# Kernel tuning notes

Hardware: AMD Instinct MI355X
Metric: run time of the kernel (lower is better)

The kernel has to match this reference:

```python
import jax, jax.numpy as jnp
import numpy as np

B, N, K, H, L = 2, 1024, 48, 128, 3
SCALE = 30.0


def _gelu(x):
    # torch.nn.GELU default is the exact erf formulation
    return jax.nn.gelu(x, approximate=False)


def _ln(x, g, b, eps=1e-5):
    mu = jnp.mean(x, axis=-1, keepdims=True)
    var = jnp.mean((x - mu) ** 2, axis=-1, keepdims=True)
    return g * (x - mu) * jax.lax.rsqrt(var + eps) + b


def _gather_nodes(nodes, idx):
    # nodes: [B,N,H], idx: [B,N,K] -> [B,N,K,H]
    b, n, k = idx.shape
    flat = idx.reshape(b, n * k)
    g = jnp.take_along_axis(nodes, flat[:, :, None], axis=1)
    return g.reshape(b, n, k, nodes.shape[-1])


def setup_inputs() -> dict:
    key = jax.random.key(0)
    ks = jax.random.split(key, 16)

    def w(k, shape, fan_in):
        return jax.random.normal(k, shape, jnp.float32) / np.sqrt(fan_in).astype(np.float32)

    kp = jax.random.split(ks[5], 9)
    inp = {
        "h_V": jax.random.normal(ks[0], (B, N, H), jnp.float32),
        "h_E": jax.random.normal(ks[1], (B, N, K, H), jnp.float32),
        "E_idx": jax.random.randint(ks[2], (B, N, K), 0, N),
        "mask_V": jnp.ones((B, N), jnp.float32),
        "mask_attend": jnp.ones((B, N, K), jnp.float32),
        # message MLP (node update): W1 [3H->H], W2, W3
        "W1": w(kp[0], (L, 3 * H, H), 3 * H), "b1": jnp.zeros((L, H), jnp.float32),
        "W2": w(kp[1], (L, H, H), H), "b2": jnp.zeros((L, H), jnp.float32),
        "W3": w(kp[2], (L, H, H), H), "b3": jnp.zeros((L, H), jnp.float32),
        # message MLP (edge update): W11 [3H->H], W12, W13
        "W11": w(kp[3], (L, 3 * H, H), 3 * H), "b11": jnp.zeros((L, H), jnp.float32),
        "W12": w(kp[4], (L, H, H), H), "b12": jnp.zeros((L, H), jnp.float32),
        "W13": w(kp[5], (L, H, H), H), "b13": jnp.zeros((L, H), jnp.float32),
        # position-wise FFN: H -> 4H -> H
        "Win": w(kp[6], (L, H, 4 * H), H), "bin_": jnp.zeros((L, 4 * H), jnp.float32),
        "Wout": w(kp[7], (L, 4 * H, H), 4 * H), "bout": jnp.zeros((L, H), jnp.float32),
        # LayerNorms
        "g1": jnp.ones((L, H), jnp.float32), "be1": jnp.zeros((L, H), jnp.float32),
        "g2": jnp.ones((L, H), jnp.float32), "be2": jnp.zeros((L, H), jnp.float32),
        "g3": jnp.ones((L, H), jnp.float32), "be3": jnp.zeros((L, H), jnp.float32),
    }
    return inp


def reference(h_V, h_E, E_idx, mask_V, mask_attend,
              W1, b1, W2, b2, W3, b3,
              W11, b11, W12, b12, W13, b13,
              Win, bin_, Wout, bout,
              g1, be1, g2, be2, g3, be3):
    # Stack of L EncLayers (eval mode, dropout = identity).
    for l in range(L):
        # --- node update: gather neighbors, concat, 3-layer MLP message ---
        hVn = _gather_nodes(h_V, E_idx)                        # [B,N,K,H]
        hVe = jnp.broadcast_to(h_V[:, :, None, :], hVn.shape)  # [B,N,K,H]
        h_EV = jnp.concatenate([hVe, h_E, hVn], axis=-1)       # [B,N,K,3H]
        m = _gelu(h_EV @ W1[l] + b1[l])
        m = _gelu(m @ W2[l] + b2[l])
        m = m @ W3[l] + b3[l]
        m = mask_attend[..., None] * m
        dh = jnp.sum(m, axis=-2) / SCALE                       # masked sum aggregate
        h_V = _ln(h_V + dh, g1[l], be1[l])
        dh = _gelu(h_V @ Win[l] + bin_[l]) @ Wout[l] + bout[l]
        h_V = _ln(h_V + dh, g2[l], be2[l])
        h_V = mask_V[..., None] * h_V
        # --- edge update ---
        hVn = _gather_nodes(h_V, E_idx)
        hVe = jnp.broadcast_to(h_V[:, :, None, :], hVn.shape)
        h_EV = jnp.concatenate([hVe, h_E, hVn], axis=-1)
        m = _gelu(h_EV @ W11[l] + b11[l])
        m = _gelu(m @ W12[l] + b12[l])
        m = m @ W13[l] + b13[l]
        h_E = _ln(h_E + m, g3[l], be3[l])
    return h_V, h_E
```

## Files before the change

kernel.cpp:

```cpp
#include <hip/hip_runtime.h>
#include <hip/hip_bf16.h>
#include <math.h>

#define BB 2
#define NN 1024
#define HH 128
#define LL 3
#define SY 136
#define SH 520
#define SX 136
#define SM 132

typedef __attribute__((ext_vector_type(8))) short s8v;
typedef __attribute__((ext_vector_type(4))) float f4v;
typedef unsigned short u16;

static __device__ __forceinline__ u16 f2bf(float x) {
  union { float f; unsigned u; } v; v.f = x;
  unsigned r = v.u + 0x7FFFu + ((v.u >> 16) & 1u);
  return (u16)(r >> 16);
}
static __device__ __forceinline__ float geluf(float x) {
  float x2 = x * x;
  float u2 = x * (1.5957691216f + 0.0713548163f * x2);
  float e = __expf(u2);
  float d = __builtin_amdgcn_rcpf(e + 1.0f);
  return x - x * d;
}

static __device__ __forceinline__ void gemm48k128(const u16* __restrict__ A,
                                                  const u16* __restrict__ Wt,
                                                  int wave, int lane, f4v acc[3][2]) {
  const int g = lane >> 4, q = lane & 15;
  s8v B0[4], B1[4];
  const u16* wb0 = Wt + (wave * 32 + q) * 128 + g * 8;
  const u16* wb1 = wb0 + 16 * 128;
#pragma unroll
  for (int t = 0; t < 4; ++t) { B0[t] = *(const s8v*)(wb0 + t * 32); B1[t] = *(const s8v*)(wb1 + t * 32); }
#pragma unroll
  for (int t = 0; t < 4; ++t) {
    const u16* Ab = A + t * 32 + g * 8;
    s8v a0 = *(const s8v*)(Ab + q * SY);
    s8v a1 = *(const s8v*)(Ab + (16 + q) * SY);
    s8v a2 = *(const s8v*)(Ab + (32 + q) * SY);
    acc[0][0] = __builtin_amdgcn_mfma_f32_16x16x32_bf16(a0, B0[t], acc[0][0], 0, 0, 0);
    acc[0][1] = __builtin_amdgcn_mfma_f32_16x16x32_bf16(a0, B1[t], acc[0][1], 0, 0, 0);
    acc[1][0] = __builtin_amdgcn_mfma_f32_16x16x32_bf16(a1, B0[t], acc[1][0], 0, 0, 0);
    acc[1][1] = __builtin_amdgcn_mfma_f32_16x16x32_bf16(a1, B1[t], acc[1][1], 0, 0, 0);
    acc[2][0] = __builtin_amdgcn_mfma_f32_16x16x32_bf16(a2, B0[t], acc[2][0], 0, 0, 0);
    acc[2][1] = __builtin_amdgcn_mfma_f32_16x16x32_bf16(a2, B1[t], acc[2][1], 0, 0, 0);
  }
}

static __device__ __forceinline__ void zero_acc(f4v acc[3][2]) {
#pragma unroll
  for (int rt = 0; rt < 3; ++rt)
#pragma unroll
    for (int c = 0; c < 2; ++c) acc[rt][c] = (f4v){0.f, 0.f, 0.f, 0.f};
}

static __device__ __forceinline__ void store_act(const f4v acc[3][2], u16* __restrict__ Y,
                                                 int wave, int lane, const float* __restrict__ bias) {
  const int g = lane >> 4, q = lane & 15;
#pragma unroll
  for (int c = 0; c < 2; ++c) {
    const int col = wave * 32 + c * 16 + q;
    const float bv = bias[col];
#pragma unroll
    for (int rt = 0; rt < 3; ++rt)
#pragma unroll
      for (int r = 0; r < 4; ++r) {
        const int row = rt * 16 + g * 4 + r;
        Y[row * SY + col] = f2bf(geluf(acc[rt][c][r] + bv));
      }
  }
}

static __device__ __forceinline__ void stage_hE(u16* __restrict__ dst, const float* __restrict__ src,
                                                int tid) {
  const float4* hEr = (const float4*)src;
#pragma unroll
  for (int p = 0; p < 6; ++p) {
    int i = tid + p * 256; int row = i >> 5, c = i & 31;
    float4 v = hEr[row * 32 + c];
    uint2 pk;
    pk.x = (unsigned)f2bf(v.x) | ((unsigned)f2bf(v.y) << 16);
    pk.y = (unsigned)f2bf(v.z) | ((unsigned)f2bf(v.w) << 16);
    *(uint2*)(dst + row * SY + c * 4) = pk;
  }
}

__global__ void conv_weights(const float* __restrict__ W1, const float* __restrict__ W2,
                             const float* __restrict__ W3, const float* __restrict__ W11,
                             const float* __restrict__ W12, const float* __restrict__ W13,
                             const float* __restrict__ Win, const float* __restrict__ Wout,
                             const float* __restrict__ hV,
                             u16* __restrict__ W1bT, u16* __restrict__ W2t,
                             u16* __restrict__ W3t, u16* __restrict__ W11bT,
                             u16* __restrict__ W12t, u16* __restrict__ W13t,
                             u16* __restrict__ Wint, u16* __restrict__ Woutt,
                             u16* __restrict__ PRE, u16* __restrict__ hv0bf) {
  const int tid = blockIdx.x * blockDim.x + threadIdx.x;
  const int nt = gridDim.x * blockDim.x;
  for (int i = tid; i < LL * 128 * 128; i += nt) {
    int l = i >> 14, rem = i & 16383;
    int k = rem >> 7, n = rem & 127;
    const int o = (l * 128 + n) * 128 + k;
    W1bT [o] = f2bf(W1 [l * 49152 + (128 + k) * 128 + n]);
    W11bT[o] = f2bf(W11[l * 49152 + (128 + k) * 128 + n]);
    W2t  [o] = f2bf(W2 [i]);
    W3t  [o] = f2bf(W3 [i]);
    W12t [o] = f2bf(W12[i]);
    W13t [o] = f2bf(W13[i]);
  }
  for (int i = tid; i < LL * 128 * 128; i += nt) {
    int l = i >> 14, rem = i & 16383;
    int k = rem >> 7, n = rem & 127;
    const int o = (l * 128 + n) * 128 + k;
    const int s = l * 16384 + k * 128 + n;
    W2t [o] = f2bf(W2 [s]);
    W3t [o] = f2bf(W3 [s]);
    W12t[o] = f2bf(W12[s]);
    W13t[o] = f2bf(W13[s]);
    const int ln = (l + 1 == LL) ? 0 : l + 1;
    PRE[l * 65536 + (0 * 128 + n) * 128 + k] = f2bf(W11[l * 49152 + k * 128 + n]);
    PRE[l * 65536 + (1 * 128 + n) * 128 + k] = f2bf(W11[l * 49152 + (256 + k) * 128 + n]);
    PRE[l * 65536 + (2 * 128 + n) * 128 + k] = f2bf(W1 [ln * 49152 + k * 128 + n]);
    PRE[l * 65536 + (3 * 128 + n) * 128 + k] = f2bf(W1 [ln * 49152 + (256 + k) * 128 + n]);
  }
  for (int i = tid; i < LL * 128 * 512; i += nt) {
    int l = i / (128 * 512), rem = i - l * 128 * 512;
    int k = rem / 512, u = rem - k * 512;
    Wint[(l * 512 + u) * 128 + k] = f2bf(Win[i]);
  }
  for (int i = tid; i < LL * 512 * 128; i += nt) {
    int l = i / (512 * 128), rem = i - l * 512 * 128;
    int k = rem / 128, n = rem - k * 128;
    Woutt[(l * 128 + n) * 512 + k] = f2bf(Wout[i]);
  }
  for (int i = tid; i < BB * NN * HH; i += nt) hv0bf[i] = f2bf(hV[i]);
}

__global__ __launch_bounds__(256) void pre_kernel(const u16* __restrict__ hvbf,
                                                  const u16* __restrict__ Wq,
                                                  const u16* __restrict__ Wp,
                                                  float* __restrict__ Q, float* __restrict__ P) {
  __shared__ __align__(16) u16 shX[16 * SX];
  const int tid = threadIdx.x, lane = tid & 63, wave = tid >> 6;
  const int g = lane >> 4, q = lane & 15;
  const int r0 = blockIdx.x * 16;
  { int row = tid >> 4, c = tid & 15;
    *(uint4*)(shX + row * SX + c * 8) = ((const uint4*)(hvbf + (size_t)r0 * 128))[tid]; }
  __syncthreads();
  s8v af[4];
#pragma unroll
  for (int t = 0; t < 4; ++t) af[t] = *(const s8v*)(shX + q * SX + t * 32 + g * 8);
  const u16* W = (wave < 2) ? Wq : Wp;
  float* D = (wave < 2) ? Q : P;
  const int c0 = (wave & 1) * 64;
#pragma unroll
  for (int cf = 0; cf < 4; ++cf) {
    const int col = c0 + cf * 16 + q;
    const u16* wb = W + (size_t)col * 128 + g * 8;
    f4v acc = (f4v){0.f, 0.f, 0.f, 0.f};
#pragma unroll
    for (int t = 0; t < 4; ++t)
      acc = __builtin_amdgcn_mfma_f32_16x16x32_bf16(af[t], *(const s8v*)(wb + t * 32), acc, 0, 0, 0);
#pragma unroll
    for (int r = 0; r < 4; ++r) D[(size_t)(r0 + g * 4 + r) * 128 + col] = acc[r];
  }
}

__global__ __launch_bounds__(256, 6) void node_msg(
    const float* __restrict__ hv_res, const float* __restrict__ Qn, const float* __restrict__ Pn,
    const float* __restrict__ hE_src, const int* __restrict__ eidx,
    const float* __restrict__ mask_att,
    const u16* __restrict__ W1bT, const u16* __restrict__ W2t, const u16* __restrict__ W3t,
    const float* __restrict__ b1, const float* __restrict__ b2, const float* __restrict__ b3,
    const float* __restrict__ g1, const float* __restrict__ be1,
    float* __restrict__ hv1, u16* __restrict__ hv1bf) {
  __shared__ __align__(16) u16 buf[2 * 48 * SY];
  __shared__ float sh_mask[48];
  __shared__ int sh_idx[48];
  __shared__ float sh_x[128];
  __shared__ float sh_st[2];
  u16* bufA = buf;
  u16* bufB = buf + 48 * SY;

  const int tid = threadIdx.x, lane = tid & 63, wave = tid >> 6;
  const int g = lane >> 4, q = lane & 15;
  const int bid = blockIdx.x, bbase = bid & ~(NN - 1);

  if (tid < 48) { sh_idx[tid] = eidx[bid * 48 + tid]; sh_mask[tid] = mask_att[bid * 48 + tid]; }
  stage_hE(bufA, hE_src + (size_t)bid * 6144, tid);
  __syncthreads();

  f4v acc[3][2];
  {
    const float* Qr = Qn + (size_t)bid * 128;
#pragma unroll
    for (int c = 0; c < 2; ++c) {
      const int col = wave * 32 + c * 16 + q;
      const float qv = Qr[col];
#pragma unroll
      for (int rt = 0; rt < 3; ++rt)
#pragma unroll
        for (int r = 0; r < 4; ++r) {
          const int row = rt * 16 + g * 4 + r;
          acc[rt][c][r] = qv + Pn[(size_t)(bbase + sh_idx[row]) * 128 + col];
        }
    }
  }
  gemm48k128(bufA, W1bT, wave, lane, acc);
  store_act(acc, bufB, wave, lane, b1);
  __syncthreads();

  zero_acc(acc);
  gemm48k128(bufB, W2t, wave, lane, acc);
  store_act(acc, bufA, wave, lane, b2);
  __syncthreads();

  zero_acc(acc);
  gemm48k128(bufA, W3t, wave, lane, acc);

  float msum = 0.f;
#pragma unroll
  for (int k = 0; k < 48; ++k) msum += sh_mask[k];
  float p0 = 0.f, p1 = 0.f;
#pragma unroll
  for (int rt = 0; rt < 3; ++rt)
#pragma unroll
    for (int r = 0; r < 4; ++r) {
      const int row = rt * 16 + g * 4 + r;
      const float mk = sh_mask[row];
      p0 += acc[rt][0][r] * mk;
      p1 += acc[rt][1][r] * mk;
    }
  p0 += __shfl_xor(p0, 16); p0 += __shfl_xor(p0, 32);
  p1 += __shfl_xor(p1, 16); p1 += __shfl_xor(p1, 32);
  if (g == 0) {
    const int c0 = wave * 32 + q, c1 = wave * 32 + 16 + q;
    sh_x[c0] = hv_res[(size_t)bid * 128 + c0] + (p0 + b3[c0] * msum) * (1.f / 30.f);
    sh_x[c1] = hv_res[(size_t)bid * 128 + c1] + (p1 + b3[c1] * msum) * (1.f / 30.f);
  }
  __syncthreads();

  if (tid < 64) {
    float a = sh_x[tid], c2 = sh_x[tid + 64];
    float s = a + c2, ss = a * a + c2 * c2;
#pragma unroll
    for (int off = 32; off; off >>= 1) { s += __shfl_xor(s, off); ss += __shfl_xor(ss, off); }
    if (tid == 0) { float mu = s * (1.f / 128.f); sh_st[0] = mu; sh_st[1] = ss * (1.f / 128.f) - mu * mu; }
  }
  __syncthreads();
  if (tid < 128) {
    float mu = sh_st[0], rs = rsqrtf(sh_st[1] + 1e-5f);
    float v = g1[tid] * (sh_x[tid] - mu) * rs + be1[tid];
    hv1[(size_t)bid * 128 + tid] = v;
    hv1bf[(size_t)bid * 128 + tid] = f2bf(v);
  }
}

__global__ __launch_bounds__(256) void ffn_kernel(
    const float* __restrict__ hv1, const u16* __restrict__ hv1bf,
    const u16* __restrict__ Wint, const float* __restrict__ binp,
    const u16* __restrict__ Woutt, const float* __restrict__ boutp,
    const float* __restrict__ g2, const float* __restrict__ be2,
    const float* __restrict__ mask_V,
    const u16* __restrict__ PRE,
    float* __restrict__ hv2,
    float* __restrict__ Qe, float* __restrict__ Pe,
    float* __restrict__ QnN, float* __restrict__ PnN) {
  __shared__ __align__(16) u16 shX[16 * SX];
  __shared__ __align__(16) u16 shH[16 * SH];
  __shared__ float shM[8 * 128];
  const int tid = threadIdx.x, lane = tid & 63, wave = tid >> 6;
  const int g = lane >> 4, q = lane & 15;
  const int r0 = blockIdx.x * 8;

  {
    int row = tid >> 4, c = tid & 15;
    uint4 v = (uint4){0, 0, 0, 0};
    if (tid < 128) v = ((const uint4*)(hv1bf + (size_t)r0 * 128))[tid];
    *(uint4*)(shX + row * SX + c * 8) = v;
  }
  __syncthreads();

  s8v a[4];
#pragma unroll
  for (int t = 0; t < 4; ++t) a[t] = *(const s8v*)(shX + q * SX + t * 32 + g * 8);
#pragma unroll
  for (int cf = 0; cf < 8; ++cf) {
    const int u = wave * 128 + cf * 16 + q;
    const u16* wb = Wint + (size_t)u * 128 + g * 8;
    f4v acc = (f4v){0.f, 0.f, 0.f, 0.f};
#pragma unroll
    for (int t = 0; t < 4; ++t)
      acc = __builtin_amdgcn_mfma_f32_16x16x32_bf16(a[t], *(const s8v*)(wb + t * 32), acc, 0, 0, 0);
    const float bv = binp[u];
#pragma unroll
    for (int r = 0; r < 4; ++r) shH[(g * 4 + r) * SH + u] = f2bf(geluf(acc[r] + bv));
  }
  __syncthreads();

#pragma unroll
  for (int c = 0; c < 2; ++c) {
    const int col = wave * 32 + c * 16 + q;
    const u16* wb = Woutt + (size_t)col * 512 + g * 8;
    s8v Bv[16];
#pragma unroll
    for (int t = 0; t < 16; ++t) Bv[t] = *(const s8v*)(wb + t * 32);
    f4v acc = (f4v){0.f, 0.f, 0.f, 0.f};
#pragma unroll
    for (int t = 0; t < 16; ++t) {
      s8v av = *(const s8v*)(shH + q * SH + t * 32 + g * 8);
      acc = __builtin_amdgcn_mfma_f32_16x16x32_bf16(av, Bv[t], acc, 0, 0, 0);
    }
    const float bv = boutp[col];
#pragma unroll
    for (int r = 0; r < 4; ++r) {
      const int row = g * 4 + r;
      if (row < 8) shM[row * 128 + col] = acc[r] + bv;
    }
  }
  __syncthreads();

#pragma unroll
  for (int i = 0; i < 2; ++i) {
    const int row = wave * 2 + i, gr = r0 + row;
    float x0 = hv1[(size_t)gr * 128 + lane]      + shM[row * 128 + lane];
    float x1 = hv1[(size_t)gr * 128 + 64 + lane] + shM[row * 128 + 64 + lane];
    float s = x0 + x1, ss = x0 * x0 + x1 * x1;
#pragma unroll
    for (int off = 32; off; off >>= 1) { s += __shfl_xor(s, off); ss += __shfl_xor(ss, off); }
    const float mu = s * (1.f / 128.f);
    const float rs = rsqrtf(ss * (1.f / 128.f) - mu * mu + 1e-5f);
    const float mv = mask_V[gr];
    float o0 = mv * (g2[lane]      * (x0 - mu) * rs + be2[lane]);
    float o1 = mv * (g2[lane + 64] * (x1 - mu) * rs + be2[lane + 64]);
    hv2[(size_t)gr * 128 + lane] = o0;
    hv2[(size_t)gr * 128 + 64 + lane] = o1;
    u16 h0 = f2bf(o0), h1 = f2bf(o1);
    shX[row * SX + lane] = h0;
    shX[row * SX + 64 + lane] = h1;
  }
  __syncthreads();

  s8v af[4];
#pragma unroll
  for (int t = 0; t < 4; ++t) af[t] = *(const s8v*)(shX + q * SX + t * 32 + g * 8);
  float* dst = (wave == 0) ? Qe : (wave == 1) ? Pe : (wave == 2) ? QnN : PnN;
  const u16* Wb = PRE + (size_t)(wave * 128) * 128;
#pragma unroll
  for (int cf = 0; cf < 8; ++cf) {
    const int colr = cf * 16 + q;
    const u16* wb = Wb + (size_t)colr * 128 + g * 8;
    f4v acc = (f4v){0.f, 0.f, 0.f, 0.f};
#pragma unroll
    for (int t = 0; t < 4; ++t)
      acc = __builtin_amdgcn_mfma_f32_16x16x32_bf16(af[t], *(const s8v*)(wb + t * 32), acc, 0, 0, 0);
    if (g < 2) {
#pragma unroll
      for (int r = 0; r < 4; ++r)
        dst[(size_t)(r0 + g * 4 + r) * 128 + colr] = acc[r];
    }
  }
}

__global__ __launch_bounds__(256, 6) void edge_kernel(
    const float* __restrict__ Qe, const float* __restrict__ Pe,
    const float* __restrict__ hE_src, const int* __restrict__ eidx,
    const u16* __restrict__ W11bT, const u16* __restrict__ W12t, const u16* __restrict__ W13t,
    const float* __restrict__ b11, const float* __restrict__ b12, const float* __restrict__ b13,
    const float* __restrict__ g3, const float* __restrict__ be3,
    float* __restrict__ hE_out) {
  __shared__ __align__(16) u16 buf[2 * 48 * SY];
  __shared__ int sh_idx[48];
  u16* bufA = buf;
  u16* bufB = buf + 48 * SY;

  const int tid = threadIdx.x, lane = tid & 63, wave = tid >> 6;
  const int g = lane >> 4, q = lane & 15;
  const int bid = blockIdx.x, bbase = bid & ~(NN - 1);

  if (tid < 48) sh_idx[tid] = eidx[bid * 48 + tid];
  stage_hE(bufA, hE_src + (size_t)bid * 6144, tid);
  __syncthreads();

  f4v acc[3][2];
  {
    const float* Qr = Qe + (size_t)bid * 128;
#pragma unroll
    for (int c = 0; c < 2; ++c) {
      const int col = wave * 32 + c * 16 + q;
      const float qv = Qr[col];
#pragma unroll
      for (int rt = 0; rt < 3; ++rt)
#pragma unroll
        for (int r = 0; r < 4; ++r) {
          const int row = rt * 16 + g * 4 + r;
          acc[rt][c][r] = qv + Pe[(size_t)(bbase + sh_idx[row]) * 128 + col];
        }
    }
  }
  gemm48k128(bufA, W11bT, wave, lane, acc);
  store_act(acc, bufB, wave, lane, b11);
  __syncthreads();

  zero_acc(acc);
  gemm48k128(bufB, W12t, wave, lane, acc);
  store_act(acc, bufA, wave, lane, b12);
  __syncthreads();

  zero_acc(acc);
  gemm48k128(bufA, W13t, wave, lane, acc);
  __syncthreads();

  float* shMf = (float*)buf;
#pragma unroll
  for (int c = 0; c < 2; ++c) {
    const int col = wave * 32 + c * 16 + q;
    const float bv = b13[col];
#pragma unroll
    for (int rt = 0; rt < 3; ++rt)
#pragma unroll
      for (int r = 0; r < 4; ++r)
        shMf[(rt * 16 + g * 4 + r) * SM + col] = acc[rt][c][r] + bv;
  }
  __syncthreads();

  const float* heb = hE_src + (size_t)bid * 6144;
  float* hob = hE_out + (size_t)bid * 6144;
#pragma unroll 1
  for (int i = 0; i < 12; ++i) {
    const int row = wave * 12 + i;
    float x0 = heb[row * 128 + lane]      + shMf[row * SM + lane];
    float x1 = heb[row * 128 + 64 + lane] + shMf[row * SM + 64 + lane];
    float s = x0 + x1, ss = x0 * x0 + x1 * x1;
#pragma unroll
    for (int off = 32; off; off >>= 1) { s += __shfl_xor(s, off); ss += __shfl_xor(ss, off); }
    const float mu = s * (1.f / 128.f);
    const float rs = rsqrtf(ss * (1.f / 128.f) - mu * mu + 1e-5f);
    hob[row * 128 + lane]      = g3[lane]      * (x0 - mu) * rs + be3[lane];
    hob[row * 128 + 64 + lane] = g3[lane + 64] * (x1 - mu) * rs + be3[lane + 64];
  }
}

extern "C" void kernel_launch(void* const* d_in, const int* in_sizes, int n_in,
                              void* d_out, int out_size, void* d_ws, size_t ws_size,
                              hipStream_t stream) {
  const float* h_V      = (const float*)d_in[0];
  const float* h_E      = (const float*)d_in[1];
  const int*   E_idx    = (const int*)d_in[2];
  const float* mask_V   = (const float*)d_in[3];
  const float* mask_att = (const float*)d_in[4];
  const float* W1   = (const float*)d_in[5];   const float* b1   = (const float*)d_in[6];
  const float* W2   = (const float*)d_in[7];   const float* b2   = (const float*)d_in[8];
  const float* W3   = (const float*)d_in[9];   const float* b3   = (const float*)d_in[10];
  const float* W11  = (const float*)d_in[11];  const float* b11  = (const float*)d_in[12];
  const float* W12  = (const float*)d_in[13];  const float* b12  = (const float*)d_in[14];
  const float* W13  = (const float*)d_in[15];  const float* b13  = (const float*)d_in[16];
  const float* Win  = (const float*)d_in[17];  const float* binp = (const float*)d_in[18];
  const float* Wout = (const float*)d_in[19];  const float* boutp= (const float*)d_in[20];
  const float* g1   = (const float*)d_in[21];  const float* be1  = (const float*)d_in[22];
  const float* g2   = (const float*)d_in[23];  const float* be2  = (const float*)d_in[24];
  const float* g3   = (const float*)d_in[25];  const float* be3  = (const float*)d_in[26];

  float* outV = (float*)d_out;
  float* outE = outV + (size_t)BB * NN * HH;

  u16* ws     = (u16*)d_ws;
  u16* W1bT   = ws;
  u16* W11bT  = W1bT  + 3 * 16384;
  u16* W2t    = W11bT + 3 * 16384;
  u16* W3t    = W2t   + 3 * 16384;
  u16* W12t   = W3t   + 3 * 16384;
  u16* W13t   = W12t  + 3 * 16384;
  u16* Wint   = W13t  + 3 * 16384;
  u16* Woutt  = Wint  + 3 * 65536;
  u16* PREb   = Woutt + 3 * 65536;
  u16* hv0bf  = PREb  + 3 * 65536;
  u16* Pbf    = hv0bf + BB * NN * HH;
  float* Pf   = (float*)(Pbf + BB * NN * HH);
  float* Qf   = Pf  + BB * NN * HH;
  float* Qn   = Qf  + BB * NN * HH;
  float* Pn   = Qn  + BB * NN * HH;
  float* Qe   = Pn  + BB * NN * HH;
  float* Pe   = Qe  + BB * NN * HH;

  conv_weights<<<512, 256, 0, stream>>>(W1, W2, W3, W11, W12, W13, Win, Wout, h_V,
                                        W1bT, W2t, W3t, W11bT, W12t, W13t, Wint, Woutt,
                                        PREb, hv0bf);

  pre_kernel<<<(BB * NN) / 16, 256, 0, stream>>>(
      hv0bf, PREb + 2 * 65536 + 2 * 16384, PREb + 2 * 65536 + 3 * 16384, Qn, Pn);

  for (int l = 0; l < LL; ++l) {
    const float* hv_res  = (l == 0) ? h_V : Qf;
    const float* hE_src  = (l == 0) ? h_E : outE;
    float*       hv2_dst = (l == 2) ? outV : Qf;

    node_msg<<<BB * NN, 256, 0, stream>>>(
        hv_res, Qn, Pn, hE_src, E_idx, mask_att,
        W1bT + l * 16384, W2t + l * 16384, W3t + l * 16384,
        b1 + l * 128, b2 + l * 128, b3 + l * 128,
        g1 + l * 128, be1 + l * 128,
        Pf, Pbf);

    ffn_kernel<<<(BB * NN) / 8, 256, 0, stream>>>(
        Pf, Pbf,
        Wint + l * 65536, binp + l * 512,
        Woutt + l * 65536, boutp + l * 128,
        g2 + l * 128, be2 + l * 128, mask_V,
        PREb + l * 65536,
        hv2_dst, Qe, Pe, Qn, Pn);

    edge_kernel<<<BB * NN, 256, 0, stream>>>(
        Qe, Pe, hE_src, E_idx,
        W11bT + l * 16384, W12t + l * 16384, W13t + l * 16384,
        b11 + l * 128, b12 + l * 128, b13 + l * 128,
        g3 + l * 128, be3 + l * 128,
        outE);
  }
}
```

Measured before the change: 326.2 us.

## Process two nodes per block with prefetched edge tiles in node and edge kernels

Node-message and edge kernels now handle two nodes per block and use a third shared buffer. The next node's h_E tile and gathered P/Q values are prefetched into registers while the current node's GEMMs run. The edge LayerNorm is rewritten to work on MFMA accumulator registers, with row statistics reduced through shared memory, so the fp32 message no longer round-trips through LDS. Occupancy bounds drop from 6 to 4 blocks per CU and the grid is halved, trading parallelism for latency hiding and higher register and LDS use.

```diff
diff --git a/kernel.cpp b/kernel.cpp
--- a/kernel.cpp
+++ b/kernel.cpp
@@ -9,7 +9,7 @@
 #define SY 136
 #define SH 520
 #define SX 136
-#define SM 132
+#define NPB 2
 
 typedef __attribute__((ext_vector_type(8))) short s8v;
 typedef __attribute__((ext_vector_type(4))) float f4v;
@@ -28,15 +28,19 @@
   return x - x * d;
 }
 
-static __device__ __forceinline__ void gemm48k128(const u16* __restrict__ A,
-                                                  const u16* __restrict__ Wt,
-                                                  int wave, int lane, f4v acc[3][2]) {
-  const int g = lane >> 4, q = lane & 15;
-  s8v B0[4], B1[4];
+static __device__ __forceinline__ void loadB(const u16* __restrict__ Wt, int wave, int lane,
+                                             s8v B0[4], s8v B1[4]) {
+  const int g = lane >> 4, q = lane & 15;
   const u16* wb0 = Wt + (wave * 32 + q) * 128 + g * 8;
   const u16* wb1 = wb0 + 16 * 128;
 #pragma unroll
   for (int t = 0; t < 4; ++t) { B0[t] = *(const s8v*)(wb0 + t * 32); B1[t] = *(const s8v*)(wb1 + t * 32); }
+}
+
+static __device__ __forceinline__ void gemmA(const u16* __restrict__ A,
+                                             const s8v B0[4], const s8v B1[4],
+                                             int lane, f4v acc[3][2]) {
+  const int g = lane >> 4, q = lane & 15;
 #pragma unroll
   for (int t = 0; t < 4; ++t) {
     const u16* Ab = A + t * 32 + g * 8;
@@ -82,12 +86,41 @@
 #pragma unroll
   for (int p = 0; p < 6; ++p) {
     int i = tid + p * 256; int row = i >> 5, c = i & 31;
-    float4 v = hEr[row * 32 + c];
+    float4 v = hEr[i];
     uint2 pk;
     pk.x = (unsigned)f2bf(v.x) | ((unsigned)f2bf(v.y) << 16);
     pk.y = (unsigned)f2bf(v.z) | ((unsigned)f2bf(v.w) << 16);
     *(uint2*)(dst + row * SY + c * 4) = pk;
   }
+}
+static __device__ __forceinline__ void stage_regs(u16* __restrict__ dst, const float4 h[6], int tid) {
+#pragma unroll
+  for (int p = 0; p < 6; ++p) {
+    int i = tid + p * 256; int row = i >> 5, c = i & 31;
+    uint2 pk;
+    pk.x = (unsigned)f2bf(h[p].x) | ((unsigned)f2bf(h[p].y) << 16);
+    pk.y = (unsigned)f2bf(h[p].z) | ((unsigned)f2bf(h[p].w) << 16);
+    *(uint2*)(dst + row * SY + c * 4) = pk;
+  }
+}
+
+static __device__ __forceinline__ void load_pq(float pP[3][4][2], float qv[2],
+                                               const float* __restrict__ Q, const float* __restrict__ P,
+                                               const int* __restrict__ eidx, int bid, int bbase,
+                                               int wave, int g, int q) {
+  const float* Qr = Q + (size_t)bid * 128;
+#pragma unroll
+  for (int c = 0; c < 2; ++c) qv[c] = Qr[wave * 32 + c * 16 + q];
+#pragma unroll
+  for (int rt = 0; rt < 3; ++rt)
+#pragma unroll
+    for (int r = 0; r < 4; ++r) {
+      const int row = rt * 16 + g * 4 + r;
+      const int idx = eidx[bid * 48 + row];
+      const float* Pr = P + (size_t)(bbase + idx) * 128 + wave * 32;
+#pragma unroll
+      for (int c = 0; c < 2; ++c) pP[rt][r][c] = Pr[c * 16 + q];
+    }
 }
 
 __global__ void conv_weights(const float* __restrict__ W1, const float* __restrict__ W2,
@@ -106,18 +139,9 @@
     int l = i >> 14, rem = i & 16383;
     int k = rem >> 7, n = rem & 127;
     const int o = (l * 128 + n) * 128 + k;
+    const int s = l * 16384 + k * 128 + n;
     W1bT [o] = f2bf(W1 [l * 49152 + (128 + k) * 128 + n]);
     W11bT[o] = f2bf(W11[l * 49152 + (128 + k) * 128 + n]);
-    W2t  [o] = f2bf(W2 [i]);
-    W3t  [o] = f2bf(W3 [i]);
-    W12t [o] = f2bf(W12[i]);
-    W13t [o] = f2bf(W13[i]);
-  }
-  for (int i = tid; i < LL * 128 * 128; i += nt) {
-    int l = i >> 14, rem = i & 16383;
-    int k = rem >> 7, n = rem & 127;
-    const int o = (l * 128 + n) * 128 + k;
-    const int s = l * 16384 + k * 128 + n;
     W2t [o] = f2bf(W2 [s]);
     W3t [o] = f2bf(W3 [s]);
     W12t[o] = f2bf(W12[s]);
@@ -171,7 +195,7 @@
   }
 }
 
-__global__ __launch_bounds__(256, 6) void node_msg(
+__global__ __launch_bounds__(256, 4) void node_msg(
     const float* __restrict__ hv_res, const float* __restrict__ Qn, const float* __restrict__ Pn,
     const float* __restrict__ hE_src, const int* __restrict__ eidx,
     const float* __restrict__ mask_att,
@@ -179,85 +203,92 @@
     const float* __restrict__ b1, const float* __restrict__ b2, const float* __restrict__ b3,
     const float* __restrict__ g1, const float* __restrict__ be1,
     float* __restrict__ hv1, u16* __restrict__ hv1bf) {
-  __shared__ __align__(16) u16 buf[2 * 48 * SY];
-  __shared__ float sh_mask[48];
-  __shared__ int sh_idx[48];
-  __shared__ float sh_x[128];
-  __shared__ float sh_st[2];
-  u16* bufA = buf;
-  u16* bufB = buf + 48 * SY;
+  __shared__ __align__(16) u16 S0[48 * SY], S1[48 * SY], Yb[48 * SY];
+  __shared__ float sh_mask[NPB * 48];
 
   const int tid = threadIdx.x, lane = tid & 63, wave = tid >> 6;
   const int g = lane >> 4, q = lane & 15;
-  const int bid = blockIdx.x, bbase = bid & ~(NN - 1);
-
-  if (tid < 48) { sh_idx[tid] = eidx[bid * 48 + tid]; sh_mask[tid] = mask_att[bid * 48 + tid]; }
-  stage_hE(bufA, hE_src + (size_t)bid * 6144, tid);
-  __syncthreads();
-
-  f4v acc[3][2];
-  {
-    const float* Qr = Qn + (size_t)bid * 128;
-#pragma unroll
-    for (int c = 0; c < 2; ++c) {
-      const int col = wave * 32 + c * 16 + q;
-      const float qv = Qr[col];
+  const int bid0 = blockIdx.x * NPB, bbase = bid0 & ~(NN - 1);
+
+  if (tid < NPB * 48) sh_mask[tid] = mask_att[bid0 * 48 + tid];
+  stage_hE(S0, hE_src + (size_t)bid0 * 6144, tid);
+  float pP[3][4][2], qv[2];
+  load_pq(pP, qv, Qn, Pn, eidx, bid0, bbase, wave, g, q);
+  __syncthreads();
+
+#pragma unroll
+  for (int i = 0; i < NPB; ++i) {
+    u16* Scur = (i == 0) ? S0 : S1;
+    u16* Snxt = (i == 0) ? S1 : S0;
+    const int bid = bid0 + i;
+
+    s8v Ba[4], Bb[4];
+    loadB(W1bT, wave, lane, Ba, Bb);
+    f4v acc[3][2];
+#pragma unroll
+    for (int c = 0; c < 2; ++c)
 #pragma unroll
       for (int rt = 0; rt < 3; ++rt)
 #pragma unroll
-        for (int r = 0; r < 4; ++r) {
-          const int row = rt * 16 + g * 4 + r;
-          acc[rt][c][r] = qv + Pn[(size_t)(bbase + sh_idx[row]) * 128 + col];
-        }
-    }
-  }
-  gemm48k128(bufA, W1bT, wave, lane, acc);
-  store_act(acc, bufB, wave, lane, b1);
-  __syncthreads();
-
-  zero_acc(acc);
-  gemm48k128(bufB, W2t, wave, lane, acc);
-  store_act(acc, bufA, wave, lane, b2);
-  __syncthreads();
-
-  zero_acc(acc);
-  gemm48k128(bufA, W3t, wave, lane, acc);
-
-  float msum = 0.f;
-#pragma unroll
-  for (int k = 0; k < 48; ++k) msum += sh_mask[k];
-  float p0 = 0.f, p1 = 0.f;
-#pragma unroll
-  for (int rt = 0; rt < 3; ++rt)
-#pragma unroll
-    for (int r = 0; r < 4; ++r) {
-      const int row = rt * 16 + g * 4 + r;
-      const float mk = sh_mask[row];
-      p0 += acc[rt][0][r] * mk;
-      p1 += acc[rt][1][r] * mk;
-    }
-  p0 += __shfl_xor(p0, 16); p0 += __shfl_xor(p0, 32);
-  p1 += __shfl_xor(p1, 16); p1 += __shfl_xor(p1, 32);
-  if (g == 0) {
-    const int c0 = wave * 32 + q, c1 = wave * 32 + 16 + q;
-    sh_x[c0] = hv_res[(size_t)bid * 128 + c0] + (p0 + b3[c0] * msum) * (1.f / 30.f);
-    sh_x[c1] = hv_res[(size_t)bid * 128 + c1] + (p1 + b3[c1] * msum) * (1.f / 30.f);
-  }
-  __syncthreads();
-
-  if (tid < 64) {
-    float a = sh_x[tid], c2 = sh_x[tid + 64];
-    float s = a + c2, ss = a * a + c2 * c2;
-#pragma unroll
-    for (int off = 32; off; off >>= 1) { s += __shfl_xor(s, off); ss += __shfl_xor(ss, off); }
-    if (tid == 0) { float mu = s * (1.f / 128.f); sh_st[0] = mu; sh_st[1] = ss * (1.f / 128.f) - mu * mu; }
-  }
-  __syncthreads();
-  if (tid < 128) {
-    float mu = sh_st[0], rs = rsqrtf(sh_st[1] + 1e-5f);
-    float v = g1[tid] * (sh_x[tid] - mu) * rs + be1[tid];
-    hv1[(size_t)bid * 128 + tid] = v;
-    hv1bf[(size_t)bid * 128 + tid] = f2bf(v);
+        for (int r = 0; r < 4; ++r) acc[rt][c][r] = qv[c] + pP[rt][r][c];
+    gemmA(Scur, Ba, Bb, lane, acc);
+
+    float4 hpre[6];
+    if (i + 1 < NPB) {
+      const float4* src = (const float4*)(hE_src + (size_t)(bid + 1) * 6144);
+#pragma unroll
+      for (int p = 0; p < 6; ++p) hpre[p] = src[tid + p * 256];
+    }
+    loadB(W2t, wave, lane, Ba, Bb);
+    __syncthreads();
+    store_act(acc, Yb, wave, lane, b1);
+    __syncthreads();
+    if (i + 1 < NPB) stage_regs(Snxt, hpre, tid);
+    zero_acc(acc);
+    gemmA(Yb, Ba, Bb, lane, acc);
+    loadB(W3t, wave, lane, Ba, Bb);
+    store_act(acc, Scur, wave, lane, b2);
+    __syncthreads();
+    zero_acc(acc);
+    gemmA(Scur, Ba, Bb, lane, acc);
+    if (i + 1 < NPB) load_pq(pP, qv, Qn, Pn, eidx, bid + 1, bbase, wave, g, q);
+
+    float msum = 0.f;
+#pragma unroll
+    for (int k = 0; k < 48; ++k) msum += sh_mask[i * 48 + k];
+    float p0 = 0.f, p1 = 0.f;
+#pragma unroll
+    for (int rt = 0; rt < 3; ++rt)
+#pragma unroll
+      for (int r = 0; r < 4; ++r) {
+        const float mk = sh_mask[i * 48 + rt * 16 + g * 4 + r];
+        p0 += acc[rt][0][r] * mk;
+        p1 += acc[rt][1][r] * mk;
+      }
+    p0 += __shfl_xor(p0, 16); p0 += __shfl_xor(p0, 32);
+    p1 += __shfl_xor(p1, 16); p1 += __shfl_xor(p1, 32);
+    float* sh_x = (float*)Yb;
+    float* sh_st = (float*)Yb + 128;
+    if (g == 0) {
+      const int c0 = wave * 32 + q, c1 = wave * 32 + 16 + q;
+      sh_x[c0] = hv_res[(size_t)bid * 128 + c0] + (p0 + b3[c0] * msum) * (1.f / 30.f);
+      sh_x[c1] = hv_res[(size_t)bid * 128 + c1] + (p1 + b3[c1] * msum) * (1.f / 30.f);
+    }
+    __syncthreads();
+    if (tid < 64) {
+      float a = sh_x[tid], c2 = sh_x[tid + 64];
+      float s = a + c2, ss = a * a + c2 * c2;
+#pragma unroll
+      for (int off = 32; off; off >>= 1) { s += __shfl_xor(s, off); ss += __shfl_xor(ss, off); }
+      if (tid == 0) { float mu = s * (1.f / 128.f); sh_st[0] = mu; sh_st[1] = ss * (1.f / 128.f) - mu * mu; }
+    }
+    __syncthreads();
+    if (tid < 128) {
+      float mu = sh_st[0], rs = rsqrtf(sh_st[1] + 1e-5f);
+      float v = g1[tid] * (sh_x[tid] - mu) * rs + be1[tid];
+      hv1[(size_t)bid * 128 + tid] = v;
+      hv1bf[(size_t)bid * 128 + tid] = f2bf(v);
+    }
   }
 }
 
@@ -340,9 +371,8 @@
     float o1 = mv * (g2[lane + 64] * (x1 - mu) * rs + be2[lane + 64]);
     hv2[(size_t)gr * 128 + lane] = o0;
     hv2[(size_t)gr * 128 + 64 + lane] = o1;
-    u16 h0 = f2bf(o0), h1 = f2bf(o1);
-    shX[row * SX + lane] = h0;
-    shX[row * SX + 64 + lane] = h1;
+    shX[row * SX + lane] = f2bf(o0);
+    shX[row * SX + 64 + lane] = f2bf(o1);
   }
   __syncthreads();
 
@@ -367,82 +397,112 @@
   }
 }
 
-__global__ __launch_bounds__(256, 6) void edge_kernel(
+__global__ __launch_bounds__(256, 4) void edge_kernel(
     const float* __restrict__ Qe, const float* __restrict__ Pe,
     const float* __restrict__ hE_src, const int* __restrict__ eidx,
     const u16* __restrict__ W11bT, const u16* __restrict__ W12t, const u16* __restrict__ W13t,
     const float* __restrict__ b11, const float* __restrict__ b12, const float* __restrict__ b13,
     const float* __restrict__ g3, const float* __restrict__ be3,
     float* __restrict__ hE_out) {
-  __shared__ __align__(16) u16 buf[2 * 48 * SY];
-  __shared__ int sh_idx[48];
-  u16* bufA = buf;
-  u16* bufB = buf + 48 * SY;
+  __shared__ __align__(16) u16 S0[48 * SY], S1[48 * SY], Yb[48 * SY];
 
   const int tid = threadIdx.x, lane = tid & 63, wave = tid >> 6;
   const int g = lane >> 4, q = lane & 15;
-  const int bid = blockIdx.x, bbase = bid & ~(NN - 1);
-
-  if (tid < 48) sh_idx[tid] = eidx[bid * 48 + tid];
-  stage_hE(bufA, hE_src + (size_t)bid * 6144, tid);
-  __syncthreads();
-
-  f4v acc[3][2];
-  {
-    const float* Qr = Qe + (size_t)bid * 128;
-#pragma unroll
-    for (int c = 0; c < 2; ++c) {
-      const int col = wave * 32 + c * 16 + q;
-      const float qv = Qr[col];
+  const int bid0 = blockIdx.x * NPB, bbase = bid0 & ~(NN - 1);
+
+  stage_hE(S0, hE_src + (size_t)bid0 * 6144, tid);
+  float pP[3][4][2], qv[2];
+  load_pq(pP, qv, Qe, Pe, eidx, bid0, bbase, wave, g, q);
+  __syncthreads();
+
+#pragma unroll
+  for (int i = 0; i < NPB; ++i) {
+    u16* Scur = (i == 0) ? S0 : S1;
+    u16* Snxt = (i == 0) ? S1 : S0;
+    const int bid = bid0 + i;
+
+    s8v Ba[4], Bb[4];
+    loadB(W11bT, wave, lane, Ba, Bb);
+    f4v acc[3][2];
+#pragma unroll
+    for (int c = 0; c < 2; ++c)
 #pragma unroll
       for (int rt = 0; rt < 3; ++rt)
 #pragma unroll
-        for (int r = 0; r < 4; ++r) {
-          const int row = rt * 16 + g * 4 + r;
-          acc[rt][c][r] = qv + Pe[(size_t)(bbase + sh_idx[row]) * 128 + col];
-        }
-    }
-  }
-  gemm48k128(bufA, W11bT, wave, lane, acc);
-  store_act(acc, bufB, wave, lane, b11);
-  __syncthreads();
-
-  zero_acc(acc);
-  gemm48k128(bufB, W12t, wave, lane, acc);
-  store_act(acc, bufA, wave, lane, b12);
-  __syncthreads();
-
-  zero_acc(acc);
-  gemm48k128(bufA, W13t, wave, lane, acc);
-  __syncthreads();
-
-  float* shMf = (float*)buf;
-#pragma unroll
-  for (int c = 0; c < 2; ++c) {
-    const int col = wave * 32 + c * 16 + q;
-    const float bv = b13[col];
+        for (int r = 0; r < 4; ++r) acc[rt][c][r] = qv[c] + pP[rt][r][c];
+    gemmA(Scur, Ba, Bb, lane, acc);
+
+    float4 hpre[6];
+    if (i + 1 < NPB) {
+      const float4* src = (const float4*)(hE_src + (size_t)(bid + 1) * 6144);
+#pragma unroll
+      for (int p = 0; p < 6; ++p) hpre[p] = src[tid + p * 256];
+    }
+    loadB(W12t, wave, lane, Ba, Bb);
+    __syncthreads();
+    store_act(acc, Yb, wave, lane, b11);
+    __syncthreads();
+    if (i + 1 < NPB) stage_regs(Snxt, hpre, tid);
+    zero_acc(acc);
+    gemmA(Yb, Ba, Bb, lane, acc);
+    loadB(W13t, wave, lane, Ba, Bb);
+    store_act(acc, Scur, wave, lane, b12);
+    __syncthreads();
+    const float* heb = hE_src + (size_t)bid * 6144;
+    float xh[3][2][4];
 #pragma unroll
     for (int rt = 0; rt < 3; ++rt)
 #pragma unroll
-      for (int r = 0; r < 4; ++r)
-        shMf[(rt * 16 + g * 4 + r) * SM + col] = acc[rt][c][r] + bv;
-  }
-  __syncthreads();
-
-  const float* heb = hE_src + (size_t)bid * 6144;
-  float* hob = hE_out + (size_t)bid * 6144;
-#pragma unroll 1
-  for (int i = 0; i < 12; ++i) {
-    const int row = wave * 12 + i;
-    float x0 = heb[row * 128 + lane]      + shMf[row * SM + lane];
-    float x1 = heb[row * 128 + 64 + lane] + shMf[row * SM + 64 + lane];
-    float s = x0 + x1, ss = x0 * x0 + x1 * x1;
-#pragma unroll
-    for (int off = 32; off; off >>= 1) { s += __shfl_xor(s, off); ss += __shfl_xor(ss, off); }
-    const float mu = s * (1.f / 128.f);
-    const float rs = rsqrtf(ss * (1.f / 128.f) - mu * mu + 1e-5f);
-    hob[row * 128 + lane]      = g3[lane]      * (x0 - mu) * rs + be3[lane];
-    hob[row * 128 + 64 + lane] = g3[lane + 64] * (x1 - mu) * rs + be3[lane + 64];
+      for (int c = 0; c < 2; ++c)
+#pragma unroll
+        for (int r = 0; r < 4; ++r)
+          xh[rt][c][r] = heb[(rt * 16 + g * 4 + r) * 128 + wave * 32 + c * 16 + q];
+    zero_acc(acc);
+    gemmA(Scur, Ba, Bb, lane, acc);
+    const float bv0 = b13[wave * 32 + q], bv1 = b13[wave * 32 + 16 + q];
+#pragma unroll
+    for (int rt = 0; rt < 3; ++rt)
+#pragma unroll
+      for (int r = 0; r < 4; ++r) {
+        xh[rt][0][r] += acc[rt][0][r] + bv0;
+        xh[rt][1][r] += acc[rt][1][r] + bv1;
+      }
+    if (i + 1 < NPB) load_pq(pP, qv, Qe, Pe, eidx, bid + 1, bbase, wave, g, q);
+
+    float2* stats = (float2*)Yb;
+    float2* statsF = stats + 192;
+#pragma unroll
+    for (int rt = 0; rt < 3; ++rt)
+#pragma unroll
+      for (int r = 0; r < 4; ++r) {
+        float s = xh[rt][0][r] + xh[rt][1][r];
+        float ss = xh[rt][0][r] * xh[rt][0][r] + xh[rt][1][r] * xh[rt][1][r];
+#pragma unroll
+        for (int off = 1; off < 16; off <<= 1) { s += __shfl_xor(s, off); ss += __shfl_xor(ss, off); }
+        if (q == 0) stats[(rt * 16 + g * 4 + r) * 4 + wave] = make_float2(s, ss);
+      }
+    __syncthreads();
+    if (tid < 48) {
+      float s = 0.f, ss = 0.f;
+#pragma unroll
+      for (int w = 0; w < 4; ++w) { float2 v = stats[tid * 4 + w]; s += v.x; ss += v.y; }
+      float mu = s * (1.f / 128.f);
+      float rs = rsqrtf(ss * (1.f / 128.f) - mu * mu + 1e-5f);
+      statsF[tid] = make_float2(mu, rs);
+    }
+    __syncthreads();
+    float* hob = hE_out + (size_t)bid * 6144;
+    const float g30 = g3[wave * 32 + q], g31 = g3[wave * 32 + 16 + q];
+    const float be30 = be3[wave * 32 + q], be31 = be3[wave * 32 + 16 + q];
+#pragma unroll
+    for (int rt = 0; rt < 3; ++rt)
+#pragma unroll
+      for (int r = 0; r < 4; ++r) {
+        const int row = rt * 16 + g * 4 + r;
+        const float2 mf = statsF[row];
+        hob[row * 128 + wave * 32 + q]      = g30 * (xh[rt][0][r] - mf.x) * mf.y + be30;
+        hob[row * 128 + wave * 32 + 16 + q] = g31 * (xh[rt][1][r] - mf.x) * mf.y + be31;
+      }
   }
 }
 
@@ -500,7 +560,7 @@
     const float* hE_src  = (l == 0) ? h_E : outE;
     float*       hv2_dst = (l == 2) ? outV : Qf;
 
-    node_msg<<<BB * NN, 256, 0, stream>>>(
+    node_msg<<<(BB * NN) / NPB, 256, 0, stream>>>(
         hv_res, Qn, Pn, hE_src, E_idx, mask_att,
         W1bT + l * 16384, W2t + l * 16384, W3t + l * 16384,
         b1 + l * 128, b2 + l * 128, b3 + l * 128,
@@ -515,7 +575,7 @@
         PREb + l * 65536,
         hv2_dst, Qe, Pe, Qn, Pn);
 
-    edge_kernel<<<BB * NN, 256, 0, stream>>>(
+    edge_kernel<<<(BB * NN) / NPB, 256, 0, stream>>>(
         Qe, Pe, hE_src, E_idx,
         W11bT + l * 16384, W12t + l * 16384, W13t + l * 16384,
         b11 + l * 128, b12 + l * 128, b13 + l * 128,
```

Result: slower. 344.2 us (+5.5%).
